# Kernel tuning notes

Hardware: AMD Instinct MI355X
Metric: run time of the kernel (lower is better)

The kernel has to match this reference:

```python
import jax, jax.numpy as jnp
import numpy as np

N = 100000   # nodes
E = 1600000  # edges (avg degree 16)
D = 32       # feature / hidden dim


def setup_inputs() -> dict:
    key = jax.random.key(0)
    k_x, k_e, kq, kk, kv, ko = jax.random.split(key, 6)
    s = 1.0 / np.sqrt(D).astype(np.float32)
    x = jax.random.normal(k_x, (N, D), dtype=jnp.float32)
    edge_index = jax.random.randint(k_e, (2, E), 0, N, dtype=jnp.int64)
    Wq = jax.random.normal(kq, (D, D), dtype=jnp.float32) * s
    Wk = jax.random.normal(kk, (D, D), dtype=jnp.float32) * s
    Wv = jax.random.normal(kv, (D, D), dtype=jnp.float32) * s
    Wo = jax.random.normal(ko, (D, D), dtype=jnp.float32) * s
    return {"x": x, "edge_index": edge_index, "Wq": Wq, "Wk": Wk, "Wv": Wv, "Wo": Wo}


def reference(x, edge_index, Wq, Wk, Wv, Wo):
    sender, receiver = edge_index[0], edge_index[1]
    n = x.shape[0]
    scale = x.shape[1] ** -0.5  # hidden_dim == D
    Q = x @ Wq  # [N, D]
    K = x @ Wk
    V = x @ Wv
    # per-edge attention scores
    scores = jnp.sum(Q[receiver] * K[sender], axis=1) * scale  # [E]
    # numerically-stable segment softmax over incoming edges of each receiver
    smax = jax.ops.segment_max(scores, receiver, num_segments=n)  # [N]
    alpha = jnp.exp(scores - smax[receiver])  # [E]
    Z = jax.ops.segment_sum(alpha, receiver, num_segments=n)  # [N]
    alpha = alpha / (Z[receiver] + 1e-6)
    # weighted aggregation of sender values
    out = jax.ops.segment_sum(alpha[:, None] * V[sender], receiver, num_segments=n)  # [N, D]
    return x + out @ Wo
```

## Files before the change

kernel.cpp:

```cpp
#include <hip/hip_runtime.h>
#include <hip/hip_bf16.h>

#define DIM 32
#define RCR 512
#define NCMAX 256
#define PBLK 256
#define SUBCAP 80
#define REGSZ (PBLK * SUBCAP)
#define CAPC 9216
#define QROWS 32

__device__ __forceinline__ float b2f(ushort h) {
    union { float f; unsigned u; } u; u.u = ((unsigned)h) << 16; return u.f;
}
__device__ __forceinline__ float h2f(ushort u) {
    _Float16 h; __builtin_memcpy(&h, &u, 2); return (float)h;
}
__device__ __forceinline__ ushort f2h(float f) {
    _Float16 h = (_Float16)f; ushort u; __builtin_memcpy(&u, &h, 2); return u;
}
__device__ __forceinline__ int load_idx(const int* __restrict__ idx, size_t pos,
                                        int mode, int n) {
    int v = mode ? idx[2 * pos] : idx[pos];
    return v < 0 ? 0 : (v >= n ? n - 1 : v);
}
__device__ __forceinline__ float load_f(const void* p, size_t i, int bf) {
    return bf ? b2f(((const ushort*)p)[i]) : ((const float*)p)[i];
}

union K1Smem {
    struct { float sW[3][DIM * DIM]; float sx[QROWS][36]; } qkv;
    struct { int h[NCMAX]; } place;
};

__global__ void __launch_bounds__(256)
qkv_place_kernel(const void* __restrict__ x_, const int* __restrict__ idx,
                 const void* __restrict__ Wq_, const void* __restrict__ Wk_,
                 const void* __restrict__ Wv_, int N, int E, int nc,
                 ushort* __restrict__ Q, ushort* __restrict__ KV,
                 unsigned* __restrict__ bedges, int* __restrict__ hcnt) {
    __shared__ K1Smem sm;
    __shared__ int sBf, sMode;

    const int tid = threadIdx.x;
    if (tid < 64) {
        int e = (((const ushort*)x_)[2 * tid] >> 7) & 0xFF;
        unsigned long long bb = __ballot(e >= 100 && e <= 135);
        unsigned long long mm = __ballot(idx[2 * tid + 1] != 0);
        if (tid == 0) { sBf = (__popcll(bb) >= 56); sMode = (mm == 0ULL); }
    }
    __syncthreads();
    const int bf = sBf, mode = sMode;

    if (blockIdx.x < PBLK) {
        const int pb = blockIdx.x;
        for (int i = tid; i < nc; i += 256) sm.place.h[i] = 0;
        __syncthreads();
        const int per = (E + PBLK - 1) / PBLK;
        const int e0 = pb * per;
        const int e1 = min(e0 + per, E);
        for (int e = e0 + tid; e < e1; e += 256) {
            const int r = load_idx(idx, (size_t)E + e, mode, N);
            const int s = load_idx(idx, (size_t)e, mode, N);
            const int cb = r >> 9;
            const int p = atomicAdd(&sm.place.h[cb], 1);
            if (p < SUBCAP)
                bedges[(size_t)cb * REGSZ + pb * SUBCAP + p] =
                    (unsigned)s | ((unsigned)(r & (RCR - 1)) << 17);
        }
        __syncthreads();
        for (int i = tid; i < nc; i += 256)
            hcnt[i * PBLK + pb] = min(sm.place.h[i], SUBCAP);
        return;
    }

    for (int i = tid; i < DIM * DIM; i += 256) {
        sm.qkv.sW[0][i] = load_f(Wq_, i, bf);
        sm.qkv.sW[1][i] = load_f(Wk_, i, bf);
        sm.qkv.sW[2][i] = load_f(Wv_, i, bf);
    }
    const int base = (blockIdx.x - PBLK) * QROWS;
    for (int i = tid; i < QROWS * DIM; i += 256) {
        const int r = i >> 5, cdim = i & 31;
        const int row = base + r;
        sm.qkv.sx[r][cdim] = (row < N) ? load_f(x_, (size_t)row * DIM + cdim, bf) : 0.f;
    }
    __syncthreads();

    const int lr  = tid >> 3;
    const int d4  = (tid & 7) * 4;
    const int row = base + lr;
    if (row >= N) return;

    float aq[4] = {0.f, 0.f, 0.f, 0.f};
    float ak[4] = {0.f, 0.f, 0.f, 0.f};
    float av[4] = {0.f, 0.f, 0.f, 0.f};
#pragma unroll
    for (int k0 = 0; k0 < DIM; k0 += 4) {
        const float4 xq = *(const float4*)&sm.qkv.sx[lr][k0];
        const float xs[4] = {xq.x, xq.y, xq.z, xq.w};
#pragma unroll
        for (int kk = 0; kk < 4; ++kk) {
            const float xv = xs[kk];
            const float4 wq = *(const float4*)&sm.qkv.sW[0][(k0 + kk) * DIM + d4];
            const float4 wk = *(const float4*)&sm.qkv.sW[1][(k0 + kk) * DIM + d4];
            const float4 wv = *(const float4*)&sm.qkv.sW[2][(k0 + kk) * DIM + d4];
            aq[0] = fmaf(xv, wq.x, aq[0]); aq[1] = fmaf(xv, wq.y, aq[1]);
            aq[2] = fmaf(xv, wq.z, aq[2]); aq[3] = fmaf(xv, wq.w, aq[3]);
            ak[0] = fmaf(xv, wk.x, ak[0]); ak[1] = fmaf(xv, wk.y, ak[1]);
            ak[2] = fmaf(xv, wk.z, ak[2]); ak[3] = fmaf(xv, wk.w, ak[3]);
            av[0] = fmaf(xv, wv.x, av[0]); av[1] = fmaf(xv, wv.y, av[1]);
            av[2] = fmaf(xv, wv.z, av[2]); av[3] = fmaf(xv, wv.w, av[3]);
        }
    }
    const float s = 0.17677669529663687f;
    ushort4 qs, ks, vs;
    qs.x = f2h(aq[0] * s); qs.y = f2h(aq[1] * s);
    qs.z = f2h(aq[2] * s); qs.w = f2h(aq[3] * s);
    ks.x = f2h(ak[0]); ks.y = f2h(ak[1]); ks.z = f2h(ak[2]); ks.w = f2h(ak[3]);
    vs.x = f2h(av[0]); vs.y = f2h(av[1]); vs.z = f2h(av[2]); vs.w = f2h(av[3]);
    *(ushort4*)&Q[(size_t)row * DIM + d4]       = qs;
    *(ushort4*)&KV[(size_t)row * 64 + d4]       = ks;
    *(ushort4*)&KV[(size_t)row * 64 + 32 + d4]  = vs;
}

__global__ void __launch_bounds__(1024)
rsort_kernel(unsigned* __restrict__ bedges, const int* __restrict__ hcnt,
             int* __restrict__ rbase, int* __restrict__ rcount, int N) {
    __shared__ unsigned eL[CAPC];
    __shared__ int cnt[RCR];
    __shared__ int fills[PBLK];
    __shared__ int cbase[PBLK];
    __shared__ int wsum[8];

    const int tid = threadIdx.x;
    const int c = blockIdx.x;
    const size_t s0 = (size_t)c * REGSZ;

    if (tid < RCR) cnt[tid] = 0;
    for (int i = tid; i < PBLK; i += 1024) fills[i] = hcnt[c * PBLK + i];
    __syncthreads();

    int fv = 0, fx = 0;
    {
        const int lane0 = tid & 63, w0 = tid >> 6;
        if (tid < PBLK) {
            fv = fills[tid]; fx = fv;
#pragma unroll
            for (int o = 1; o < 64; o <<= 1) {
                int t = __shfl_up(fx, o); if (lane0 >= o) fx += t;
            }
            if (lane0 == 63) wsum[w0] = fx;
        }
    }
    __syncthreads();
    if (tid == 0) {
        int a = 0;
#pragma unroll
        for (int k = 0; k < 4; ++k) { int t = wsum[k]; wsum[k] = a; a += t; }
    }
    __syncthreads();
    if (tid < PBLK) cbase[tid] = fx - fv + wsum[tid >> 6];
    __syncthreads();
    const int nTot = cbase[PBLK - 1] + fills[PBLK - 1];

    for (int i = tid; i < REGSZ; i += 1024) {
        const int cell = i / SUBCAP;
        const int q    = i - cell * SUBCAP;
        if (q < fills[cell]) {
            const int p = cbase[cell] + q;
            if (p < CAPC) {
                const unsigned e = bedges[s0 + i];
                eL[p] = e;
                atomicAdd(&cnt[(e >> 17) & (RCR - 1)], 1);
            }
        }
    }
    __syncthreads();

    const int lane = tid & 63, w = tid >> 6;
    const int v = (tid < RCR) ? cnt[tid] : 0;
    int x = v;
#pragma unroll
    for (int o = 1; o < 64; o <<= 1) {
        int t = __shfl_up(x, o); if (lane >= o) x += t;
    }
    if (tid < RCR && lane == 63) wsum[w] = x;
    __syncthreads();
    if (tid == 0) {
        int a = 0;
#pragma unroll
        for (int k = 0; k < 8; ++k) { int t = wsum[k]; wsum[k] = a; a += t; }
    }
    __syncthreads();
    int excl = 0;
    if (tid < RCR) {
        excl = x - v + wsum[w];
        rbase[c * RCR + tid]  = (int)s0 + excl;
        rcount[c * RCR + tid] = v;
    }
    __syncthreads();
    if (tid < RCR) cnt[tid] = (int)s0 + excl;
    __syncthreads();

    const int m = min(nTot, CAPC);
    for (int i = tid; i < m; i += 1024) {
        const unsigned e = eL[i];
        const int p = atomicAdd(&cnt[(e >> 17) & (RCR - 1)], 1);
        bedges[p] = e & 0x1FFFF;
    }
}

__global__ void __launch_bounds__(256)
agg_kernel(const ushort* __restrict__ Q, const ushort* __restrict__ KV,
           const unsigned* __restrict__ bedges, const int* __restrict__ rbase,
           const int* __restrict__ rcount, const void* __restrict__ x_,
           const void* __restrict__ Wo_, int N, float* __restrict__ out) {
    __shared__ float sWo[DIM * DIM];
    __shared__ float accS[32][DIM + 1];
    __shared__ float Zs[32];
    __shared__ unsigned sQ[32 * 16];
    __shared__ int sBf;

    const int tid = threadIdx.x;
    if (tid < 64) {
        int e = (((const ushort*)x_)[2 * tid] >> 7) & 0xFF;
        unsigned long long bb = __ballot(e >= 100 && e <= 135);
        if (tid == 0) sBf = (__popcll(bb) >= 56);
    }
    const int r0 = blockIdx.x * 32;
    const int nr = min(32, N - r0);
    __syncthreads();
    const int bf = sBf;

    for (int i = tid; i < DIM * DIM; i += 256) sWo[i] = load_f(Wo_, i, bf);
    for (int i = tid; i < nr * 16; i += 256)
        sQ[i] = ((const unsigned*)(Q + (size_t)r0 * DIM))[i];
    __syncthreads();

    const int w    = tid >> 6;
    const int lane = tid & 63;
    const int i8   = lane >> 3;
    const int j    = lane & 7;

    for (int t = w; t < nr; t += 8) {
        const int rlA = t;
        const int rlB = t + 4;
        const bool hasB = (rlB < nr);

        const int degA = rcount[r0 + rlA];
        const int o0A  = rbase[r0 + rlA];
        const int degB = hasB ? rcount[r0 + rlB] : 0;
        const int o0B  = hasB ? rbase[r0 + rlB] : o0A;

        const ushort4 qa = *(const ushort4*)((const ushort*)sQ + rlA * DIM + j * 4);
        const ushort4 qb = *(const ushort4*)((const ushort*)sQ + (rlB & 31) * DIM + j * 4);
        const float qA0 = h2f(qa.x), qA1 = h2f(qa.y), qA2 = h2f(qa.z), qA3 = h2f(qa.w);
        const float qB0 = h2f(qb.x), qB1 = h2f(qb.y), qB2 = h2f(qb.z), qB3 = h2f(qb.w);

        float axA = 0.f, ayA = 0.f, azA = 0.f, awA = 0.f, zsA = 0.f;
        float axB = 0.f, ayB = 0.f, azB = 0.f, awB = 0.f, zsB = 0.f;

        const int chA = (degA + 7) >> 3;
        const int chB = (degB + 7) >> 3;
        const int cmax = max(chA, chB);
        const int dmA = max(degA - 1, 0);
        const int dmB = max(degB - 1, 0);

        for (int cc = 0; cc < cmax; cc += 2) {
            const int c0 = cc * 8 + i8;
            const int c1 = c0 + 8;
            const bool okA0 = (c0 < degA), okA1 = (c1 < degA);
            const bool okB0 = (c0 < degB), okB1 = (c1 < degB);

            const int sA0 = (int)bedges[o0A + (okA0 ? c0 : dmA)];
            const int sA1 = (int)bedges[o0A + (okA1 ? c1 : dmA)];
            const int sB0 = (int)bedges[o0B + (okB0 ? c0 : dmB)];
            const int sB1 = (int)bedges[o0B + (okB1 ? c1 : dmB)];

            const ushort* pA0 = KV + (size_t)sA0 * 64;
            const ushort* pA1 = KV + (size_t)sA1 * 64;
            const ushort* pB0 = KV + (size_t)sB0 * 64;
            const ushort* pB1 = KV + (size_t)sB1 * 64;

            const ushort4 khA0 = *(const ushort4*)(pA0 + j * 4);
            const ushort4 vhA0 = *(const ushort4*)(pA0 + 32 + j * 4);
            const ushort4 khA1 = *(const ushort4*)(pA1 + j * 4);
            const ushort4 vhA1 = *(const ushort4*)(pA1 + 32 + j * 4);
            const ushort4 khB0 = *(const ushort4*)(pB0 + j * 4);
            const ushort4 vhB0 = *(const ushort4*)(pB0 + 32 + j * 4);
            const ushort4 khB1 = *(const ushort4*)(pB1 + j * 4);
            const ushort4 vhB1 = *(const ushort4*)(pB1 + 32 + j * 4);

            float pA = h2f(khA0.x) * qA0;
            float pAx = h2f(khA1.x) * qA0;
            float pB = h2f(khB0.x) * qB0;
            float pBx = h2f(khB1.x) * qB0;
            pA  = fmaf(h2f(khA0.y), qA1, pA);   pAx = fmaf(h2f(khA1.y), qA1, pAx);
            pB  = fmaf(h2f(khB0.y), qB1, pB);   pBx = fmaf(h2f(khB1.y), qB1, pBx);
            pA  = fmaf(h2f(khA0.z), qA2, pA);   pAx = fmaf(h2f(khA1.z), qA2, pAx);
            pB  = fmaf(h2f(khB0.z), qB2, pB);   pBx = fmaf(h2f(khB1.z), qB2, pBx);
            pA  = fmaf(h2f(khA0.w), qA3, pA);   pAx = fmaf(h2f(khA1.w), qA3, pAx);
            pB  = fmaf(h2f(khB0.w), qB3, pB);   pBx = fmaf(h2f(khB1.w), qB3, pBx);

            pA  += __shfl_xor(pA, 1);   pAx += __shfl_xor(pAx, 1);
            pB  += __shfl_xor(pB, 1);   pBx += __shfl_xor(pBx, 1);
            pA  += __shfl_xor(pA, 2);   pAx += __shfl_xor(pAx, 2);
            pB  += __shfl_xor(pB, 2);   pBx += __shfl_xor(pBx, 2);
            pA  += __shfl_xor(pA, 4);   pAx += __shfl_xor(pAx, 4);
            pB  += __shfl_xor(pB, 4);   pBx += __shfl_xor(pBx, 4);

            pA  = fminf(fmaxf(pA,  -60.f), 60.f);
            pAx = fminf(fmaxf(pAx, -60.f), 60.f);
            pB  = fminf(fmaxf(pB,  -60.f), 60.f);
            pBx = fminf(fmaxf(pBx, -60.f), 60.f);
            const float aA0 = okA0 ? __expf(pA)  : 0.f;
            const float aA1 = okA1 ? __expf(pAx) : 0.f;
            const float aB0 = okB0 ? __expf(pB)  : 0.f;
            const float aB1 = okB1 ? __expf(pBx) : 0.f;

            axA = fmaf(h2f(vhA0.x), aA0, axA);  axA = fmaf(h2f(vhA1.x), aA1, axA);
            ayA = fmaf(h2f(vhA0.y), aA0, ayA);  ayA = fmaf(h2f(vhA1.y), aA1, ayA);
            azA = fmaf(h2f(vhA0.z), aA0, azA);  azA = fmaf(h2f(vhA1.z), aA1, azA);
            awA = fmaf(h2f(vhA0.w), aA0, awA);  awA = fmaf(h2f(vhA1.w), aA1, awA);
            zsA += aA0 + aA1;

            axB = fmaf(h2f(vhB0.x), aB0, axB);  axB = fmaf(h2f(vhB1.x), aB1, axB);
            ayB = fmaf(h2f(vhB0.y), aB0, ayB);  ayB = fmaf(h2f(vhB1.y), aB1, ayB);
            azB = fmaf(h2f(vhB0.z), aB0, azB);  azB = fmaf(h2f(vhB1.z), aB1, azB);
            awB = fmaf(h2f(vhB0.w), aB0, awB);  awB = fmaf(h2f(vhB1.w), aB1, awB);
            zsB += aB0 + aB1;
        }

#pragma unroll
        for (int o = 8; o < 64; o <<= 1) {
            axA += __shfl_xor(axA, o); ayA += __shfl_xor(ayA, o);
            azA += __shfl_xor(azA, o); awA += __shfl_xor(awA, o);
            zsA += __shfl_xor(zsA, o);
            axB += __shfl_xor(axB, o); ayB += __shfl_xor(ayB, o);
            azB += __shfl_xor(azB, o); awB += __shfl_xor(awB, o);
            zsB += __shfl_xor(zsB, o);
        }
        if (i8 == 0) {
            float* arA = accS[rlA];
            arA[j * 4 + 0] = axA; arA[j * 4 + 1] = ayA;
            arA[j * 4 + 2] = azA; arA[j * 4 + 3] = awA;
            if (j == 0) Zs[rlA] = zsA;
            if (hasB) {
                float* arB = accS[rlB];
                arB[j * 4 + 0] = axB; arB[j * 4 + 1] = ayB;
                arB[j * 4 + 2] = azB; arB[j * 4 + 3] = awB;
                if (j == 0) Zs[rlB] = zsB;
            }
        }
    }
    __syncthreads();

    const int lr = tid >> 5;
    const int d  = tid & 31;
#pragma unroll
    for (int it = 0; it < 4; ++it) {
        const int rl = it * 8 + lr;
        if (rl < nr) {
            const float inv = 1.f / (Zs[rl] + 1e-6f);
            float o = 0.f;
#pragma unroll
            for (int k = 0; k < DIM; ++k) o += accS[rl][k] * sWo[k * DIM + d];
            const size_t oi = (size_t)(r0 + rl) * DIM + d;
            out[oi] = load_f(x_, oi, bf) + inv * o;
        }
    }
}

extern "C" void kernel_launch(void* const* d_in, const int* in_sizes, int n_in,
                              void* d_out, int out_size, void* d_ws, size_t ws_size,
                              hipStream_t stream) {
    const void* x   = d_in[0];
    const int*  idx = (const int*)d_in[1];
    const void* Wq  = d_in[2];
    const void* Wk  = d_in[3];
    const void* Wv  = d_in[4];
    const void* Wo  = d_in[5];
    float* out = (float*)d_out;

    const int N = in_sizes[0] / DIM;
    const int E = in_sizes[1] / 2;
    const int nc = (N + RCR - 1) / RCR;
    const size_t N32 = (size_t)N * DIM;

    ushort*   Q      = (ushort*)d_ws;
    ushort*   KV     = Q + N32;
    unsigned* bedges = (unsigned*)(KV + (size_t)N * 64);
    int*      hcnt   = (int*)(bedges + (size_t)nc * REGSZ);
    int*      rbase  = hcnt + (size_t)nc * PBLK;
    int*      rcount = rbase + (size_t)nc * RCR;

    const int qkv_blocks = (N + QROWS - 1) / QROWS;
    qkv_place_kernel<<<PBLK + qkv_blocks, 256, 0, stream>>>(
        x, idx, Wq, Wk, Wv, N, E, nc, Q, KV, bedges, hcnt);

    rsort_kernel<<<nc, 1024, 0, stream>>>(bedges, hcnt, rbase, rcount, N);

    agg_kernel<<<(N + 31) / 32, 256, 0, stream>>>(Q, KV, bedges, rbase,
                                                  rcount, x, Wo, N, out);
}
```

Measured before the change: 182.6 us.

## Shrink receiver regions to 128 rows and run bucket sort with 256 threads

Cuts the receiver-region size from 512 to 128 rows and the placement partitions from 256 to 128 blocks. Per-cell capacity and the shared sort buffer shrink with it, so there are more, smaller rsort blocks of 256 threads, and the scan logic is reworked for the smaller widths. The aim is better occupancy and load balance in the sort stage, with smaller per-block LDS use and fewer wasted slots in the padded bucket regions. It also vectorises the x loads in the QKV projection. The tighter capacities (48 per sub-cell, 2816 per region) risk dropping edges when degree varies, and the placement histogram is now 782 entries per block.

```diff
diff --git a/kernel.cpp b/kernel.cpp
--- a/kernel.cpp
+++ b/kernel.cpp
@@ -1,14 +1,12 @@
 #include <hip/hip_runtime.h>
-#include <hip/hip_bf16.h>
 
 #define DIM 32
-#define RCR 512
-#define NCMAX 256
-#define PBLK 256
-#define SUBCAP 80
+#define RCR 128
+#define NCMAX 1024
+#define PBLK 128
+#define SUBCAP 48
 #define REGSZ (PBLK * SUBCAP)
-#define CAPC 9216
-#define QROWS 32
+#define CAPC 2816
 
 __device__ __forceinline__ float b2f(ushort h) {
     union { float f; unsigned u; } u; u.u = ((unsigned)h) << 16; return u.f;
@@ -18,18 +16,21 @@
 }
 __device__ __forceinline__ ushort f2h(float f) {
     _Float16 h = (_Float16)f; ushort u; __builtin_memcpy(&u, &h, 2); return u;
+}
+__device__ __forceinline__ int clampN(int v, int n) {
+    return v < 0 ? 0 : (v >= n ? n - 1 : v);
 }
 __device__ __forceinline__ int load_idx(const int* __restrict__ idx, size_t pos,
                                         int mode, int n) {
     int v = mode ? idx[2 * pos] : idx[pos];
-    return v < 0 ? 0 : (v >= n ? n - 1 : v);
+    return clampN(v, n);
 }
 __device__ __forceinline__ float load_f(const void* p, size_t i, int bf) {
     return bf ? b2f(((const ushort*)p)[i]) : ((const float*)p)[i];
 }
 
 union K1Smem {
-    struct { float sW[3][DIM * DIM]; float sx[QROWS][36]; } qkv;
+    struct { float sW[3][DIM * DIM]; float sx[32][36]; } g;
     struct { int h[NCMAX]; } place;
 };
 
@@ -62,11 +63,12 @@
         for (int e = e0 + tid; e < e1; e += 256) {
             const int r = load_idx(idx, (size_t)E + e, mode, N);
             const int s = load_idx(idx, (size_t)e, mode, N);
-            const int cb = r >> 9;
-            const int p = atomicAdd(&sm.place.h[cb], 1);
+            const int reg = r >> 7;
+            const int rl  = r & (RCR - 1);
+            const int p = atomicAdd(&sm.place.h[reg], 1);
             if (p < SUBCAP)
-                bedges[(size_t)cb * REGSZ + pb * SUBCAP + p] =
-                    (unsigned)s | ((unsigned)(r & (RCR - 1)) << 17);
+                bedges[(size_t)reg * REGSZ + pb * SUBCAP + p] =
+                    (unsigned)s | ((unsigned)rl << 17);
         }
         __syncthreads();
         for (int i = tid; i < nc; i += 256)
@@ -75,20 +77,31 @@
     }
 
     for (int i = tid; i < DIM * DIM; i += 256) {
-        sm.qkv.sW[0][i] = load_f(Wq_, i, bf);
-        sm.qkv.sW[1][i] = load_f(Wk_, i, bf);
-        sm.qkv.sW[2][i] = load_f(Wv_, i, bf);
-    }
-    const int base = (blockIdx.x - PBLK) * QROWS;
-    for (int i = tid; i < QROWS * DIM; i += 256) {
-        const int r = i >> 5, cdim = i & 31;
+        sm.g.sW[0][i] = load_f(Wq_, i, bf);
+        sm.g.sW[1][i] = load_f(Wk_, i, bf);
+        sm.g.sW[2][i] = load_f(Wv_, i, bf);
+    }
+    const int base = (blockIdx.x - PBLK) * 32;
+    for (int i = tid; i < 32 * 8; i += 256) {
+        const int r  = i >> 3;
+        const int c4 = (i & 7) << 2;
         const int row = base + r;
-        sm.qkv.sx[r][cdim] = (row < N) ? load_f(x_, (size_t)row * DIM + cdim, bf) : 0.f;
+        float4 v; v.x = v.y = v.z = v.w = 0.f;
+        if (row < N) {
+            if (!bf) {
+                v = *(const float4*)((const float*)x_ + (size_t)row * DIM + c4);
+            } else {
+                const ushort4 u =
+                    *(const ushort4*)((const ushort*)x_ + (size_t)row * DIM + c4);
+                v.x = b2f(u.x); v.y = b2f(u.y); v.z = b2f(u.z); v.w = b2f(u.w);
+            }
+        }
+        *(float4*)&sm.g.sx[r][c4] = v;
     }
     __syncthreads();
 
     const int lr  = tid >> 3;
-    const int d4  = (tid & 7) * 4;
+    const int d4  = (tid & 7) << 2;
     const int row = base + lr;
     if (row >= N) return;
 
@@ -97,14 +110,14 @@
     float av[4] = {0.f, 0.f, 0.f, 0.f};
 #pragma unroll
     for (int k0 = 0; k0 < DIM; k0 += 4) {
-        const float4 xq = *(const float4*)&sm.qkv.sx[lr][k0];
+        const float4 xq = *(const float4*)&sm.g.sx[lr][k0];
         const float xs[4] = {xq.x, xq.y, xq.z, xq.w};
 #pragma unroll
         for (int kk = 0; kk < 4; ++kk) {
             const float xv = xs[kk];
-            const float4 wq = *(const float4*)&sm.qkv.sW[0][(k0 + kk) * DIM + d4];
-            const float4 wk = *(const float4*)&sm.qkv.sW[1][(k0 + kk) * DIM + d4];
-            const float4 wv = *(const float4*)&sm.qkv.sW[2][(k0 + kk) * DIM + d4];
+            const float4 wq = *(const float4*)&sm.g.sW[0][(k0 + kk) * DIM + d4];
+            const float4 wk = *(const float4*)&sm.g.sW[1][(k0 + kk) * DIM + d4];
+            const float4 wv = *(const float4*)&sm.g.sW[2][(k0 + kk) * DIM + d4];
             aq[0] = fmaf(xv, wq.x, aq[0]); aq[1] = fmaf(xv, wq.y, aq[1]);
             aq[2] = fmaf(xv, wq.z, aq[2]); aq[3] = fmaf(xv, wq.w, aq[3]);
             ak[0] = fmaf(xv, wk.x, ak[0]); ak[1] = fmaf(xv, wk.y, ak[1]);
@@ -113,58 +126,52 @@
             av[2] = fmaf(xv, wv.z, av[2]); av[3] = fmaf(xv, wv.w, av[3]);
         }
     }
-    const float s = 0.17677669529663687f;
-    ushort4 qs, ks, vs;
-    qs.x = f2h(aq[0] * s); qs.y = f2h(aq[1] * s);
-    qs.z = f2h(aq[2] * s); qs.w = f2h(aq[3] * s);
-    ks.x = f2h(ak[0]); ks.y = f2h(ak[1]); ks.z = f2h(ak[2]); ks.w = f2h(ak[3]);
-    vs.x = f2h(av[0]); vs.y = f2h(av[1]); vs.z = f2h(av[2]); vs.w = f2h(av[3]);
-    *(ushort4*)&Q[(size_t)row * DIM + d4]       = qs;
-    *(ushort4*)&KV[(size_t)row * 64 + d4]       = ks;
-    *(ushort4*)&KV[(size_t)row * 64 + 32 + d4]  = vs;
-}
-
-__global__ void __launch_bounds__(1024)
+    const float sc = 0.17677669529663687f;
+    ushort4 t;
+    t.x = f2h(aq[0] * sc); t.y = f2h(aq[1] * sc);
+    t.z = f2h(aq[2] * sc); t.w = f2h(aq[3] * sc);
+    *(ushort4*)&Q[(size_t)row * DIM + d4] = t;
+    t.x = f2h(ak[0]); t.y = f2h(ak[1]); t.z = f2h(ak[2]); t.w = f2h(ak[3]);
+    *(ushort4*)&KV[(size_t)row * 64 + d4] = t;
+    t.x = f2h(av[0]); t.y = f2h(av[1]); t.z = f2h(av[2]); t.w = f2h(av[3]);
+    *(ushort4*)&KV[(size_t)row * 64 + 32 + d4] = t;
+}
+
+__global__ void __launch_bounds__(256)
 rsort_kernel(unsigned* __restrict__ bedges, const int* __restrict__ hcnt,
              int* __restrict__ rbase, int* __restrict__ rcount, int N) {
     __shared__ unsigned eL[CAPC];
     __shared__ int cnt[RCR];
     __shared__ int fills[PBLK];
     __shared__ int cbase[PBLK];
-    __shared__ int wsum[8];
+    __shared__ int wsum[4];
 
     const int tid = threadIdx.x;
     const int c = blockIdx.x;
     const size_t s0 = (size_t)c * REGSZ;
+    const int lane = tid & 63, w = tid >> 6;
 
     if (tid < RCR) cnt[tid] = 0;
-    for (int i = tid; i < PBLK; i += 1024) fills[i] = hcnt[c * PBLK + i];
+    if (tid < PBLK) fills[tid] = hcnt[c * PBLK + tid];
     __syncthreads();
 
     int fv = 0, fx = 0;
-    {
-        const int lane0 = tid & 63, w0 = tid >> 6;
-        if (tid < PBLK) {
-            fv = fills[tid]; fx = fv;
-#pragma unroll
-            for (int o = 1; o < 64; o <<= 1) {
-                int t = __shfl_up(fx, o); if (lane0 >= o) fx += t;
-            }
-            if (lane0 == 63) wsum[w0] = fx;
-        }
-    }
-    __syncthreads();
-    if (tid == 0) {
-        int a = 0;
-#pragma unroll
-        for (int k = 0; k < 4; ++k) { int t = wsum[k]; wsum[k] = a; a += t; }
-    }
-    __syncthreads();
-    if (tid < PBLK) cbase[tid] = fx - fv + wsum[tid >> 6];
+    if (tid < PBLK) {
+        fv = fills[tid]; fx = fv;
+#pragma unroll
+        for (int o = 1; o < 64; o <<= 1) {
+            int t = __shfl_up(fx, o); if (lane >= o) fx += t;
+        }
+        if (lane == 63) wsum[w] = fx;
+    }
+    __syncthreads();
+    if (tid == 0) { int t0 = wsum[0]; wsum[0] = 0; wsum[1] = t0; }
+    __syncthreads();
+    if (tid < PBLK) cbase[tid] = fx - fv + wsum[w];
     __syncthreads();
     const int nTot = cbase[PBLK - 1] + fills[PBLK - 1];
 
-    for (int i = tid; i < REGSZ; i += 1024) {
+    for (int i = tid; i < REGSZ; i += 256) {
         const int cell = i / SUBCAP;
         const int q    = i - cell * SUBCAP;
         if (q < fills[cell]) {
@@ -178,20 +185,17 @@
     }
     __syncthreads();
 
-    const int lane = tid & 63, w = tid >> 6;
     const int v = (tid < RCR) ? cnt[tid] : 0;
     int x = v;
-#pragma unroll
-    for (int o = 1; o < 64; o <<= 1) {
-        int t = __shfl_up(x, o); if (lane >= o) x += t;
-    }
-    if (tid < RCR && lane == 63) wsum[w] = x;
-    __syncthreads();
-    if (tid == 0) {
-        int a = 0;
-#pragma unroll
-        for (int k = 0; k < 8; ++k) { int t = wsum[k]; wsum[k] = a; a += t; }
-    }
+    if (tid < RCR) {
+#pragma unroll
+        for (int o = 1; o < 64; o <<= 1) {
+            int t = __shfl_up(x, o); if (lane >= o) x += t;
+        }
+        if (lane == 63) wsum[w] = x;
+    }
+    __syncthreads();
+    if (tid == 0) { int t0 = wsum[0]; wsum[0] = 0; wsum[1] = t0; }
     __syncthreads();
     int excl = 0;
     if (tid < RCR) {
@@ -204,7 +208,7 @@
     __syncthreads();
 
     const int m = min(nTot, CAPC);
-    for (int i = tid; i < m; i += 1024) {
+    for (int i = tid; i < m; i += 256) {
         const unsigned e = eL[i];
         const int p = atomicAdd(&cnt[(e >> 17) & (RCR - 1)], 1);
         bedges[p] = e & 0x1FFFF;
@@ -395,11 +399,11 @@
     int*      rbase  = hcnt + (size_t)nc * PBLK;
     int*      rcount = rbase + (size_t)nc * RCR;
 
-    const int qkv_blocks = (N + QROWS - 1) / QROWS;
-    qkv_place_kernel<<<PBLK + qkv_blocks, 256, 0, stream>>>(
+    const int gemm_blocks = (N + 31) / 32;
+    qkv_place_kernel<<<PBLK + gemm_blocks, 256, 0, stream>>>(
         x, idx, Wq, Wk, Wv, N, E, nc, Q, KV, bedges, hcnt);
 
-    rsort_kernel<<<nc, 1024, 0, stream>>>(bedges, hcnt, rbase, rcount, N);
+    rsort_kernel<<<nc, 256, 0, stream>>>(bedges, hcnt, rbase, rcount, N);
 
     agg_kernel<<<(N + 31) / 32, 256, 0, stream>>>(Q, KV, bedges, rbase,
                                                   rcount, x, Wo, N, out);
```

After: 191.3 us. +4.8%, slower.
